# Kernel optimization log

Measured on AMD Instinct MI355X. Metric: run time of the kernel, lower is better.

Reference implementation:

```python
import jax, jax.numpy as jnp
import numpy as np

G = 17  # groups == deform_groups
EPS = 1e-5

# regular 3x3 kernel grid in homogeneous coords: rows = (dy, dx, 1), cols = 9 kernel taps (row-major)
REG = jnp.array([[-1, -1, -1, 0, 0, 0, 1, 1, 1],
                 [-1, 0, 1, -1, 0, 1, -1, 0, 1],
                 [1, 1, 1, 1, 1, 1, 1, 1, 1]], dtype=jnp.float32)
KY = jnp.array([-1, -1, -1, 0, 0, 0, 1, 1, 1], dtype=jnp.float32)
KX = jnp.array([-1, 0, 1, -1, 0, 1, -1, 0, 1], dtype=jnp.float32)


def setup_inputs() -> dict:
    key = jax.random.key(0)
    k0, k1, k2 = jax.random.split(key, 3)
    B, C, H, W = 2, 272, 128, 128
    Cg = C // G
    x = jax.random.normal(k0, (B, C, H, W), jnp.float32)
    tm_w = jax.random.normal(k1, (6 * G, Cg, 3, 3), jnp.float32) * 0.02  # offset-transform conv weight
    tm_b = jnp.zeros((6 * G,), jnp.float32)
    dc_w = jax.random.normal(k2, (C, Cg, 3, 3), jnp.float32) * 0.05     # deform conv weight (no bias)
    gamma = jnp.ones((C,), jnp.float32)
    beta = jnp.zeros((C,), jnp.float32)
    return dict(x=x, tm_w=tm_w, tm_b=tm_b, dc_w=dc_w, gamma=gamma, beta=beta)


def _deform_sample(x, dy, dx):
    """Bilinear-sample x (B,C,H,W) at per-group offsets dy,dx (B,H,W,G,9).
    Returns (B,G,Cg,9,H,W). Zero padding outside the image (mmcv semantics)."""
    B, C, H, W = x.shape
    Cg = C // G
    hh = jnp.arange(H, dtype=x.dtype)[None, :, None, None, None]
    ww = jnp.arange(W, dtype=x.dtype)[None, None, :, None, None]
    py = hh + KY + dy  # (B,H,W,G,9)
    px = ww + KX + dx
    y0 = jnp.floor(py)
    x0 = jnp.floor(px)
    wy = py - y0
    wx = px - x0
    y0i = y0.astype(jnp.int32)
    x0i = x0.astype(jnp.int32)
    x_g = x.reshape(B, G, Cg, H * W)

    def corner(yi, xi, wgt):
        valid = (yi >= 0) & (yi < H) & (xi >= 0) & (xi < W)
        lin = jnp.clip(yi, 0, H - 1) * W + jnp.clip(xi, 0, W - 1)  # (B,H,W,G,9)
        lin = lin.transpose(0, 3, 4, 1, 2).reshape(B, G, 1, 9 * H * W)
        idx = jnp.broadcast_to(lin, (B, G, Cg, 9 * H * W))
        vals = jnp.take_along_axis(x_g, idx, axis=3).reshape(B, G, Cg, 9, H, W)
        w = (wgt * valid.astype(x.dtype)).transpose(0, 3, 4, 1, 2)  # (B,G,9,H,W)
        return vals * w[:, :, None]

    samp = corner(y0i, x0i, (1 - wy) * (1 - wx))
    samp = samp + corner(y0i, x0i + 1, (1 - wy) * wx)
    samp = samp + corner(y0i + 1, x0i, wy * (1 - wx))
    samp = samp + corner(y0i + 1, x0i + 1, wy * wx)
    return samp


def _forward(x, tm_w, tm_b, dc_w, gamma, beta):
    B, C, H, W = x.shape
    Cg = C // G
    # 1) offset-transform conv (grouped 3x3, SAME)
    aff = jax.lax.conv_general_dilated(
        x, tm_w, window_strides=(1, 1), padding='SAME',
        dimension_numbers=('NCHW', 'OIHW', 'NCHW'), feature_group_count=G)
    aff = aff + tm_b[None, :, None, None]  # (B,6G,H,W)
    # faithful to torch: view(B,2,3,G,H,W).permute(0,4,5,3,1,2) @ REG
    aff = aff.reshape(B, 2, 3, G, H, W).transpose(0, 4, 5, 3, 1, 2)  # (B,H,W,G,2,3)
    off = jnp.einsum('bhwgij,jk->bhwgik', aff, REG)  # (B,H,W,G,2,9)
    # DeformConv2d reads the flattened 18 channels as interleaved (dy,dx) pairs per tap
    off = off.reshape(B, H, W, G, 18).reshape(B, H, W, G, 9, 2)
    dy, dx = off[..., 0], off[..., 1]
    # 2) deformable 3x3 conv, groups=deform_groups=G, bias=False
    samp = _deform_sample(x, dy, dx)  # (B,G,Cg,9,H,W)
    w = dc_w.reshape(G, Cg, Cg, 3 * 3)  # (g, out-in-group, in-in-group, tap)
    out = jnp.einsum('bgckhw,gock->bgohw', samp, w).reshape(B, C, H, W)
    # 3) batch norm (training-mode stats) + residual ReLU
    mean = jnp.mean(out, axis=(0, 2, 3), keepdims=True)
    var = jnp.var(out, axis=(0, 2, 3), keepdims=True)
    out = (out - mean) * jax.lax.rsqrt(var + EPS)
    out = out * gamma[None, :, None, None] + beta[None, :, None, None]
    return jax.nn.relu(out + x)


def reference(x, tm_w, tm_b, dc_w, gamma, beta):
    return _forward(x, tm_w, tm_b, dc_w, gamma, beta)
```

## Files before the change

kernel.cpp:

```cpp
#include <hip/hip_runtime.h>
#include <math.h>

#define BB 2
#define CC 272
#define GG 17
#define CG 16
#define HH 128
#define WW 128
#define HWX (HH*WW)
#define AFFC 102
#define NSLAB (BB*GG)
#define TILES_PER_SLAB 64
#define NWG (NSLAB*TILES_PER_SLAB)
#define WGPX (NWG/8)
#define PSTR ((size_t)NSLAB*HWX*4)

typedef float f4nt __attribute__((ext_vector_type(4)));
typedef unsigned u4nt __attribute__((ext_vector_type(4)));
typedef _Float16 h2 __attribute__((ext_vector_type(2)));

__device__ __forceinline__ h2 bch(unsigned u) { return __builtin_bit_cast(h2, u); }
__device__ __forceinline__ unsigned hpk(float a, float b) {
    return __builtin_bit_cast(unsigned, __builtin_amdgcn_cvt_pkrtz(a, b));
}
__device__ __forceinline__ h2 hbc(float a) {
    return __builtin_bit_cast(h2, __builtin_amdgcn_cvt_pkrtz(a, a));
}

#if __has_builtin(__builtin_amdgcn_fdot2)
#define FDOT2(A, B, C) __builtin_amdgcn_fdot2((A), (B), (C), false)
#else
#define FDOT2(A, B, C) fmaf((float)(A).x, (float)(B).x, fmaf((float)(A).y, (float)(B).y, (C)))
#endif

__device__ __forceinline__ unsigned f2bf(float f) {
    unsigned u = __float_as_uint(f);
    return (u + 0x7fffu + ((u >> 16) & 1u)) >> 16;
}
__device__ __forceinline__ float bflo(unsigned u) { return __uint_as_float(u << 16); }
__device__ __forceinline__ float bfhi(unsigned u) { return __uint_as_float(u & 0xffff0000u); }

__global__ __launch_bounds__(256) void wt_kernel(
    const float* __restrict__ dc_w, const float* __restrict__ tm_w,
    unsigned* __restrict__ dc_wh, unsigned* __restrict__ tm_wh)
{
    int i = blockIdx.x * 256 + threadIdx.x;
    if (i < GG * 8 * 9 * CG) {
        int oc = i & 15, t = (i >> 4) % 9, cp = (i / 144) % 8, g = i / 1152;
        float w0 = dc_w[((size_t)(g * 16 + oc) * 16 + 2 * cp) * 9 + t];
        float w1 = dc_w[((size_t)(g * 16 + oc) * 16 + 2 * cp + 1) * 9 + t];
        dc_wh[i] = hpk(w0, w1);
    }
    if (i < GG * 6 * 9 * 8) {
        int cp = i & 7, t = (i >> 3) % 9, j = (i / 72) % 6, ig = i / 432;
        float w0 = tm_w[((size_t)(ig * 6 + j) * 16 + 2 * cp) * 9 + t];
        float w1 = tm_w[((size_t)(ig * 6 + j) * 16 + 2 * cp + 1) * 9 + t];
        tm_wh[i] = hpk(w0, w1);
    }
}

__global__ __launch_bounds__(256) void transpose_kernel(
    const float* __restrict__ x, unsigned* __restrict__ xt)
{
    __shared__ float tile[CG][WW + 1];
    const int h = blockIdx.x & (HH - 1);
    const int g = (blockIdx.x >> 7) % GG;
    const int b = blockIdx.x / (GG * HH);
    const int tid = threadIdx.x;
    const float* src = x + (size_t)(b * CC + g * CG) * HWX + h * WW;
    for (int i = tid; i < CG * WW; i += 256) {
        int c = i >> 7, w = i & (WW - 1);
        tile[c][w] = src[(size_t)c * HWX + w];
    }
    __syncthreads();
    const size_t rowbase = ((size_t)(b * GG + g) * HWX + h * WW) * 4;
    unsigned* d0 = xt + rowbase;
    unsigned* d1 = xt + PSTR + rowbase;
    for (int i = tid; i < 4 * WW; i += 256) {
        int w = i >> 2, c4 = i & 3;
        d0[(size_t)w * 4 + c4] = hpk(tile[2 * c4][w],     tile[2 * c4 + 1][w]);
        d1[(size_t)w * 4 + c4] = hpk(tile[8 + 2 * c4][w], tile[8 + 2 * c4 + 1][w]);
    }
}

__global__ __launch_bounds__(256) void aff_conv_kernel(
    const unsigned* __restrict__ xt, const unsigned* __restrict__ tm_wh,
    const float* __restrict__ tm_b, float* __restrict__ aff)
{
    const int ig = blockIdx.y;
    const int b = blockIdx.z;
    const int tid = threadIdx.x;

    const int p = blockIdx.x * 256 + tid;
    const int h = p >> 7, w = p & (WW - 1);
    const unsigned* xb0 = xt + (size_t)(b * GG + ig) * HWX * 4;
    const unsigned* xb1 = xb0 + PSTR;
    const unsigned* wbh = tm_wh + (size_t)ig * (6 * 9 * 8);

    float acc[6];
#pragma unroll
    for (int j = 0; j < 6; ++j) acc[j] = 0.f;

#pragma unroll 1
    for (int t = 0; t < 9; ++t) {
        int hy = h + t / 3 - 1;
        int wx = w + t % 3 - 1;
        uint4 u0 = {0, 0, 0, 0}, u1 = {0, 0, 0, 0};
        if (hy >= 0 && hy < HH && wx >= 0 && wx < WW) {
            u0 = *(const uint4*)(xb0 + (size_t)(hy * WW + wx) * 4);
            u1 = *(const uint4*)(xb1 + (size_t)(hy * WW + wx) * 4);
        }
#pragma unroll
        for (int j = 0; j < 6; ++j) {
            const uint4* wp = (const uint4*)(wbh + (j * 9 + t) * 8);
            uint4 qa = wp[0], qb = wp[1];
            float a = acc[j];
            a = FDOT2(bch(u0.x), bch(qa.x), a); a = FDOT2(bch(u0.y), bch(qa.y), a);
            a = FDOT2(bch(u0.z), bch(qa.z), a); a = FDOT2(bch(u0.w), bch(qa.w), a);
            a = FDOT2(bch(u1.x), bch(qb.x), a); a = FDOT2(bch(u1.y), bch(qb.y), a);
            a = FDOT2(bch(u1.z), bch(qb.z), a); a = FDOT2(bch(u1.w), bch(qb.w), a);
            acc[j] = a;
        }
    }
#pragma unroll
    for (int j = 0; j < 6; ++j)
        aff[(size_t)(b * AFFC + ig * 6 + j) * HWX + p] = acc[j] + tm_b[ig * 6 + j];
}


#define MACC(T, CP, S2) { \
    const uint4* wp_ = (const uint4*)(wgh + ((CP) * 9 + (T)) * CG); \
    uint4 q0 = wp_[0], q1 = wp_[1], q2 = wp_[2], q3 = wp_[3]; \
    acc[0]  = FDOT2(S2, bch(q0.x), acc[0]);  acc[1]  = FDOT2(S2, bch(q0.y), acc[1]); \
    acc[2]  = FDOT2(S2, bch(q0.z), acc[2]);  acc[3]  = FDOT2(S2, bch(q0.w), acc[3]); \
    acc[4]  = FDOT2(S2, bch(q1.x), acc[4]);  acc[5]  = FDOT2(S2, bch(q1.y), acc[5]); \
    acc[6]  = FDOT2(S2, bch(q1.z), acc[6]);  acc[7]  = FDOT2(S2, bch(q1.w), acc[7]); \
    acc[8]  = FDOT2(S2, bch(q2.x), acc[8]);  acc[9]  = FDOT2(S2, bch(q2.y), acc[9]); \
    acc[10] = FDOT2(S2, bch(q2.z), acc[10]); acc[11] = FDOT2(S2, bch(q2.w), acc[11]); \
    acc[12] = FDOT2(S2, bch(q3.x), acc[12]); acc[13] = FDOT2(S2, bch(q3.y), acc[13]); \
    acc[14] = FDOT2(S2, bch(q3.z), acc[14]); acc[15] = FDOT2(S2, bch(q3.w), acc[15]); }

#define SEM(T, CP, UA, UB, UC, UD) { \
    h2 s2 = bch(UA) * W00 + bch(UB) * W01 + bch(UC) * W10 + bch(UD) * W11; \
    MACC(T, CP, s2) }

#define TAP(T, I0, K0, I1, K1) { \
    float dy = ((I0) ? a10 : a00) * (float)((K0) / 3 - 1) \
             + ((I0) ? a11 : a01) * (float)((K0) % 3 - 1) + ((I0) ? a12 : a02); \
    float dx = ((I1) ? a10 : a00) * (float)((K1) / 3 - 1) \
             + ((I1) ? a11 : a01) * (float)((K1) % 3 - 1) + ((I1) ? a12 : a02); \
    float py = (float)(h + (T) / 3 - 1) + dy; \
    float px = (float)(w + (T) % 3 - 1) + dx; \
    float y0f = floorf(py), x0f = floorf(px); \
    float wy = py - y0f, wx = px - x0f; \
    int y0 = (int)y0f, x0 = (int)x0f; \
    int y1 = y0 + 1, x1 = x0 + 1; \
    bool vy0 = (y0 >= 0) && (y0 < HH), vy1 = (y1 >= 0) && (y1 < HH); \
    bool vx0 = (x0 >= 0) && (x0 < WW), vx1 = (x1 >= 0) && (x1 < WW); \
    int y0c = min(max(y0, 0), HH - 1), y1c = min(max(y1, 0), HH - 1); \
    int x0c = min(max(x0, 0), WW - 1), x1c = min(max(x1, 0), WW - 1); \
    float w00 = (vy0 && vx0) ? (1.f - wy) * (1.f - wx) : 0.f; \
    float w01 = (vy0 && vx1) ? (1.f - wy) * wx : 0.f; \
    float w10 = (vy1 && vx0) ? wy * (1.f - wx) : 0.f; \
    float w11 = (vy1 && vx1) ? wy * wx : 0.f; \
    h2 W00 = hbc(w00), W01 = hbc(w01), W10 = hbc(w10), W11 = hbc(w11); \
    int l00 = y0c * WW + x0c, l01 = y0c * WW + x1c; \
    int l10 = y1c * WW + x0c, l11 = y1c * WW + x1c; \
    uint4 A0 = *(const uint4*)(xb0 + (size_t)l00 * 4); \
    uint4 A1 = *(const uint4*)(xb1 + (size_t)l00 * 4); \
    uint4 B0 = *(const uint4*)(xb0 + (size_t)l01 * 4); \
    uint4 B1 = *(const uint4*)(xb1 + (size_t)l01 * 4); \
    uint4 C0 = *(const uint4*)(xb0 + (size_t)l10 * 4); \
    uint4 C1 = *(const uint4*)(xb1 + (size_t)l10 * 4); \
    uint4 D0 = *(const uint4*)(xb0 + (size_t)l11 * 4); \
    uint4 D1 = *(const uint4*)(xb1 + (size_t)l11 * 4); \
    SEM(T, 0, A0.x, B0.x, C0.x, D0.x) SEM(T, 1, A0.y, B0.y, C0.y, D0.y) \
    SEM(T, 2, A0.z, B0.z, C0.z, D0.z) SEM(T, 3, A0.w, B0.w, C0.w, D0.w) \
    SEM(T, 4, A1.x, B1.x, C1.x, D1.x) SEM(T, 5, A1.y, B1.y, C1.y, D1.y) \
    SEM(T, 6, A1.z, B1.z, C1.z, D1.z) SEM(T, 7, A1.w, B1.w, C1.w, D1.w) }

__global__ __launch_bounds__(256, 6) void deform_kernel(
    const unsigned* __restrict__ xt, const unsigned* __restrict__ dc_wh,
    const float* __restrict__ aff_buf, unsigned* __restrict__ pre,
    float* __restrict__ stat_sum, float* __restrict__ stat_sqs)
{
    __shared__ float red[CG][4][2];

    const int bid = blockIdx.x;
    const int work = (bid & 7) * WGPX + (bid >> 3);
    const int slab = work / TILES_PER_SLAB;
    const int tile = work % TILES_PER_SLAB;
    const int b = slab / GG;
    const int g = slab % GG;

    const int tid = threadIdx.y * 16 + threadIdx.x;
    const int h = (tile >> 3) * 16 + threadIdx.y;
    const int w = (tile & 7) * 16 + threadIdx.x;

    const float* ab = aff_buf + (size_t)b * AFFC * HWX + h * WW + w;
    float a00 = __builtin_nontemporal_load(ab + (size_t)(0 * 51 + 0 * 17 + g) * HWX);
    float a01 = __builtin_nontemporal_load(ab + (size_t)(0 * 51 + 1 * 17 + g) * HWX);
    float a02 = __builtin_nontemporal_load(ab + (size_t)(0 * 51 + 2 * 17 + g) * HWX);
    float a10 = __builtin_nontemporal_load(ab + (size_t)(1 * 51 + 0 * 17 + g) * HWX);
    float a11 = __builtin_nontemporal_load(ab + (size_t)(1 * 51 + 1 * 17 + g) * HWX);
    float a12 = __builtin_nontemporal_load(ab + (size_t)(1 * 51 + 2 * 17 + g) * HWX);

    const unsigned* xb0 = xt + (size_t)(b * GG + g) * HWX * 4;
    const unsigned* xb1 = xb0 + PSTR;
    const unsigned* wgh = dc_wh + (size_t)g * (8 * 9 * CG);

    float acc[CG];
#pragma unroll
    for (int oc = 0; oc < CG; ++oc) acc[oc] = 0.f;

    TAP(0, 0, 0, 0, 1)
    TAP(1, 0, 2, 0, 3)
    TAP(2, 0, 4, 0, 5)
    TAP(3, 0, 6, 0, 7)
    TAP(4, 0, 8, 1, 0)
    TAP(5, 1, 1, 1, 2)
    TAP(6, 1, 3, 1, 4)
    TAP(7, 1, 5, 1, 6)
    TAP(8, 1, 7, 1, 8)

    unsigned pk[8];
#pragma unroll
    for (int k = 0; k < 8; ++k)
        pk[k] = f2bf(acc[2 * k]) | (f2bf(acc[2 * k + 1]) << 16);
    {
        u4nt q0 = {pk[0], pk[1], pk[2], pk[3]};
        u4nt q1 = {pk[4], pk[5], pk[6], pk[7]};
        u4nt* pp = (u4nt*)(pre + ((size_t)slab * HWX + h * WW + w) * (CG / 2));
        __builtin_nontemporal_store(q0, pp);
        __builtin_nontemporal_store(q1, pp + 1);
    }

    const int lane = tid & 63, wave = tid >> 6;
#pragma unroll
    for (int oc = 0; oc < CG; ++oc) {
        float s = acc[oc], q = acc[oc] * acc[oc];
#pragma unroll
        for (int off = 32; off > 0; off >>= 1) {
            s += __shfl_down(s, off);
            q += __shfl_down(q, off);
        }
        if (lane == 0) { red[oc][wave][0] = s; red[oc][wave][1] = q; }
    }
    __syncthreads();
    if (tid < CG) {
        float s = red[tid][0][0] + red[tid][1][0] + red[tid][2][0] + red[tid][3][0];
        float q = red[tid][0][1] + red[tid][1][1] + red[tid][2][1] + red[tid][3][1];
        int ch = g * CG + tid;
        atomicAdd(&stat_sum[ch], s);
        atomicAdd(&stat_sqs[ch], q);
    }
}

__global__ __launch_bounds__(256) void bn_res_relu_kernel(
    const unsigned* __restrict__ pre, const float* __restrict__ x,
    const float* __restrict__ ssum, const float* __restrict__ ssqs,
    const float* __restrict__ gamma, const float* __restrict__ beta,
    float* __restrict__ out)
{
    const int blk = blockIdx.x;
    const int slab = blk >> 4;
    const int chunk = blk & 15;
    const int b = slab / GG, g = slab % GG;
    const int px0 = chunk * 1024 + threadIdx.x * 4;

    const float n = (float)(BB * HWX);
    float sc[16], sh[16];
#pragma unroll
    for (int oc = 0; oc < 16; ++oc) {
        int ch = g * CG + oc;
        float mean = ssum[ch] / n;
        float var = ssqs[ch] / n - mean * mean;
        float s = rsqrtf(var + 1e-5f) * gamma[ch];
        sc[oc] = s;
        sh[oc] = fmaf(-mean, s, beta[ch]);
    }

    const uint4* pp = (const uint4*)(pre + ((size_t)slab * HWX + px0) * (CG / 2));
    unsigned Pu[32];
#pragma unroll
    for (int k = 0; k < 8; ++k) {
        uint4 v = pp[k];
        Pu[4 * k] = v.x; Pu[4 * k + 1] = v.y; Pu[4 * k + 2] = v.z; Pu[4 * k + 3] = v.w;
    }
    const float* xb = x + (size_t)(b * CC + g * CG) * HWX + px0;
    float* ob = out + (size_t)(b * CC + g * CG) * HWX + px0;

#pragma unroll
    for (int oc = 0; oc < 16; ++oc) {
        f4nt xv = __builtin_nontemporal_load((const f4nt*)(xb + (size_t)oc * HWX));
        f4nt r;
        float p0, p1, p2, p3;
        {
            unsigned u0 = Pu[0 * 8 + (oc >> 1)], u1 = Pu[1 * 8 + (oc >> 1)];
            unsigned u2 = Pu[2 * 8 + (oc >> 1)], u3 = Pu[3 * 8 + (oc >> 1)];
            p0 = (oc & 1) ? bfhi(u0) : bflo(u0);
            p1 = (oc & 1) ? bfhi(u1) : bflo(u1);
            p2 = (oc & 1) ? bfhi(u2) : bflo(u2);
            p3 = (oc & 1) ? bfhi(u3) : bflo(u3);
        }
        r.x = fmaxf(fmaf(p0, sc[oc], sh[oc]) + xv.x, 0.f);
        r.y = fmaxf(fmaf(p1, sc[oc], sh[oc]) + xv.y, 0.f);
        r.z = fmaxf(fmaf(p2, sc[oc], sh[oc]) + xv.z, 0.f);
        r.w = fmaxf(fmaf(p3, sc[oc], sh[oc]) + xv.w, 0.f);
        __builtin_nontemporal_store(r, (f4nt*)(ob + (size_t)oc * HWX));
    }
}

extern "C" void kernel_launch(void* const* d_in, const int* in_sizes, int n_in,
                              void* d_out, int out_size, void* d_ws, size_t ws_size,
                              hipStream_t stream)
{
    const float* x     = (const float*)d_in[0];
    const float* tm_w  = (const float*)d_in[1];
    const float* tm_b  = (const float*)d_in[2];
    const float* dc_w  = (const float*)d_in[3];
    const float* gamma = (const float*)d_in[4];
    const float* beta  = (const float*)d_in[5];
    float* out = (float*)d_out;

    float* ws = (float*)d_ws;
    float* stat_sum = ws;
    float* stat_sqs = ws + CC;
    unsigned* dc_wh = (unsigned*)(ws + 2048);
    unsigned* tm_wh = dc_wh + 19712;
    float* aff = (float*)(tm_wh + 7424);
    unsigned* xtb = (unsigned*)(aff + (size_t)BB * AFFC * HWX);
    unsigned* preb = xtb + 2 * PSTR;

    (void)hipMemsetAsync(stat_sum, 0, 2 * CC * sizeof(float), stream);

    wt_kernel<<<dim3(77), dim3(256), 0, stream>>>(dc_w, tm_w, dc_wh, tm_wh);
    transpose_kernel<<<dim3(BB * GG * HH), dim3(256), 0, stream>>>(x, xtb);
    aff_conv_kernel<<<dim3(HWX / 256, GG, BB), dim3(256), 0, stream>>>(xtb, tm_wh, tm_b, aff);
    deform_kernel<<<dim3(NWG), dim3(16, 16), 0, stream>>>(
        xtb, dc_wh, aff, preb, stat_sum, stat_sqs);
    bn_res_relu_kernel<<<dim3(NSLAB * 16), dim3(256), 0, stream>>>(
        preb, x, stat_sum, stat_sqs, gamma, beta, out);
}
```

Baseline: 121.0 us.

## Compute two pixels per thread in deform kernel to amortize weight loads

Each deform-kernel thread now handles two pixels 16 columns apart, sharing each weight uint4 load across both accumulator sets. Tiles per slab are halved so the grid shrinks, and the launch bound drops to 4 waves to make room for the extra registers. The affine conv tap loop is also partially unrolled. The gain is fewer weight loads per output and more independent gathers in flight per thread. The cost is much higher register pressure and occupancy, plus fewer workgroups to cover the device.

```diff
diff --git a/kernel.cpp b/kernel.cpp
--- a/kernel.cpp
+++ b/kernel.cpp
@@ -10,7 +10,7 @@
 #define HWX (HH*WW)
 #define AFFC 102
 #define NSLAB (BB*GG)
-#define TILES_PER_SLAB 64
+#define TILES_PER_SLAB 32
 #define NWG (NSLAB*TILES_PER_SLAB)
 #define WGPX (NWG/8)
 #define PSTR ((size_t)NSLAB*HWX*4)
@@ -101,7 +101,7 @@
 #pragma unroll
     for (int j = 0; j < 6; ++j) acc[j] = 0.f;
 
-#pragma unroll 1
+#pragma unroll 3
     for (int t = 0; t < 9; ++t) {
         int hy = h + t / 3 - 1;
         int wx = w + t % 3 - 1;
@@ -144,42 +144,53 @@
     h2 s2 = bch(UA) * W00 + bch(UB) * W01 + bch(UC) * W10 + bch(UD) * W11; \
     MACC(T, CP, s2) }
 
-#define TAP(T, I0, K0, I1, K1) { \
-    float dy = ((I0) ? a10 : a00) * (float)((K0) / 3 - 1) \
-             + ((I0) ? a11 : a01) * (float)((K0) % 3 - 1) + ((I0) ? a12 : a02); \
-    float dx = ((I1) ? a10 : a00) * (float)((K1) / 3 - 1) \
-             + ((I1) ? a11 : a01) * (float)((K1) % 3 - 1) + ((I1) ? a12 : a02); \
-    float py = (float)(h + (T) / 3 - 1) + dy; \
-    float px = (float)(w + (T) % 3 - 1) + dx; \
-    float y0f = floorf(py), x0f = floorf(px); \
-    float wy = py - y0f, wx = px - x0f; \
-    int y0 = (int)y0f, x0 = (int)x0f; \
-    int y1 = y0 + 1, x1 = x0 + 1; \
-    bool vy0 = (y0 >= 0) && (y0 < HH), vy1 = (y1 >= 0) && (y1 < HH); \
-    bool vx0 = (x0 >= 0) && (x0 < WW), vx1 = (x1 >= 0) && (x1 < WW); \
-    int y0c = min(max(y0, 0), HH - 1), y1c = min(max(y1, 0), HH - 1); \
-    int x0c = min(max(x0, 0), WW - 1), x1c = min(max(x1, 0), WW - 1); \
-    float w00 = (vy0 && vx0) ? (1.f - wy) * (1.f - wx) : 0.f; \
-    float w01 = (vy0 && vx1) ? (1.f - wy) * wx : 0.f; \
-    float w10 = (vy1 && vx0) ? wy * (1.f - wx) : 0.f; \
-    float w11 = (vy1 && vx1) ? wy * wx : 0.f; \
-    h2 W00 = hbc(w00), W01 = hbc(w01), W10 = hbc(w10), W11 = hbc(w11); \
-    int l00 = y0c * WW + x0c, l01 = y0c * WW + x1c; \
-    int l10 = y1c * WW + x0c, l11 = y1c * WW + x1c; \
-    uint4 A0 = *(const uint4*)(xb0 + (size_t)l00 * 4); \
-    uint4 A1 = *(const uint4*)(xb1 + (size_t)l00 * 4); \
-    uint4 B0 = *(const uint4*)(xb0 + (size_t)l01 * 4); \
-    uint4 B1 = *(const uint4*)(xb1 + (size_t)l01 * 4); \
-    uint4 C0 = *(const uint4*)(xb0 + (size_t)l10 * 4); \
-    uint4 C1 = *(const uint4*)(xb1 + (size_t)l10 * 4); \
-    uint4 D0 = *(const uint4*)(xb0 + (size_t)l11 * 4); \
-    uint4 D1 = *(const uint4*)(xb1 + (size_t)l11 * 4); \
-    SEM(T, 0, A0.x, B0.x, C0.x, D0.x) SEM(T, 1, A0.y, B0.y, C0.y, D0.y) \
-    SEM(T, 2, A0.z, B0.z, C0.z, D0.z) SEM(T, 3, A0.w, B0.w, C0.w, D0.w) \
-    SEM(T, 4, A1.x, B1.x, C1.x, D1.x) SEM(T, 5, A1.y, B1.y, C1.y, D1.y) \
-    SEM(T, 6, A1.z, B1.z, C1.z, D1.z) SEM(T, 7, A1.w, B1.w, C1.w, D1.w) }
-
-__global__ __launch_bounds__(256, 6) void deform_kernel(
+template<int T, int I0, int K0, int I1, int K1>
+__device__ __forceinline__ void tap_px(
+    const unsigned* __restrict__ xb0, const unsigned* __restrict__ xb1,
+    const unsigned* __restrict__ wgh,
+    float a00, float a01, float a02, float a10, float a11, float a12,
+    int h, int w, float (&acc)[16])
+{
+    float dy = (I0 ? a10 : a00) * (float)(K0 / 3 - 1)
+             + (I0 ? a11 : a01) * (float)(K0 % 3 - 1) + (I0 ? a12 : a02);
+    float dx = (I1 ? a10 : a00) * (float)(K1 / 3 - 1)
+             + (I1 ? a11 : a01) * (float)(K1 % 3 - 1) + (I1 ? a12 : a02);
+    float py = (float)(h + T / 3 - 1) + dy;
+    float px = (float)(w + T % 3 - 1) + dx;
+    float y0f = floorf(py), x0f = floorf(px);
+    float wy = py - y0f, wx = px - x0f;
+    int y0 = (int)y0f, x0 = (int)x0f;
+    int y1 = y0 + 1, x1 = x0 + 1;
+    bool vy0 = (y0 >= 0) && (y0 < HH), vy1 = (y1 >= 0) && (y1 < HH);
+    bool vx0 = (x0 >= 0) && (x0 < WW), vx1 = (x1 >= 0) && (x1 < WW);
+    int y0c = min(max(y0, 0), HH - 1), y1c = min(max(y1, 0), HH - 1);
+    int x0c = min(max(x0, 0), WW - 1), x1c = min(max(x1, 0), WW - 1);
+    float w00 = (vy0 && vx0) ? (1.f - wy) * (1.f - wx) : 0.f;
+    float w01 = (vy0 && vx1) ? (1.f - wy) * wx : 0.f;
+    float w10 = (vy1 && vx0) ? wy * (1.f - wx) : 0.f;
+    float w11 = (vy1 && vx1) ? wy * wx : 0.f;
+    h2 W00 = hbc(w00), W01 = hbc(w01), W10 = hbc(w10), W11 = hbc(w11);
+    int l00 = y0c * WW + x0c, l01 = y0c * WW + x1c;
+    int l10 = y1c * WW + x0c, l11 = y1c * WW + x1c;
+    uint4 A0 = *(const uint4*)(xb0 + (size_t)l00 * 4);
+    uint4 A1 = *(const uint4*)(xb1 + (size_t)l00 * 4);
+    uint4 B0 = *(const uint4*)(xb0 + (size_t)l01 * 4);
+    uint4 B1 = *(const uint4*)(xb1 + (size_t)l01 * 4);
+    uint4 C0 = *(const uint4*)(xb0 + (size_t)l10 * 4);
+    uint4 C1 = *(const uint4*)(xb1 + (size_t)l10 * 4);
+    uint4 D0 = *(const uint4*)(xb0 + (size_t)l11 * 4);
+    uint4 D1 = *(const uint4*)(xb1 + (size_t)l11 * 4);
+    SEM(T, 0, A0.x, B0.x, C0.x, D0.x) SEM(T, 1, A0.y, B0.y, C0.y, D0.y)
+    SEM(T, 2, A0.z, B0.z, C0.z, D0.z) SEM(T, 3, A0.w, B0.w, C0.w, D0.w)
+    SEM(T, 4, A1.x, B1.x, C1.x, D1.x) SEM(T, 5, A1.y, B1.y, C1.y, D1.y)
+    SEM(T, 6, A1.z, B1.z, C1.z, D1.z) SEM(T, 7, A1.w, B1.w, C1.w, D1.w)
+}
+
+#define TAP2(T, I0, K0, I1, K1) \
+    tap_px<T, I0, K0, I1, K1>(xb0, xb1, wgh, a00, a01, a02, a10, a11, a12, h, w0, acc0); \
+    tap_px<T, I0, K0, I1, K1>(xb0, xb1, wgh, b00, b01, b02, b10, b11, b12, h, w1, acc1);
+
+__global__ __launch_bounds__(256, 4) void deform_kernel(
     const unsigned* __restrict__ xt, const unsigned* __restrict__ dc_wh,
     const float* __restrict__ aff_buf, unsigned* __restrict__ pre,
     float* __restrict__ stat_sum, float* __restrict__ stat_sqs)
@@ -194,51 +205,70 @@
     const int g = slab % GG;
 
     const int tid = threadIdx.y * 16 + threadIdx.x;
-    const int h = (tile >> 3) * 16 + threadIdx.y;
-    const int w = (tile & 7) * 16 + threadIdx.x;
-
-    const float* ab = aff_buf + (size_t)b * AFFC * HWX + h * WW + w;
-    float a00 = __builtin_nontemporal_load(ab + (size_t)(0 * 51 + 0 * 17 + g) * HWX);
-    float a01 = __builtin_nontemporal_load(ab + (size_t)(0 * 51 + 1 * 17 + g) * HWX);
-    float a02 = __builtin_nontemporal_load(ab + (size_t)(0 * 51 + 2 * 17 + g) * HWX);
-    float a10 = __builtin_nontemporal_load(ab + (size_t)(1 * 51 + 0 * 17 + g) * HWX);
-    float a11 = __builtin_nontemporal_load(ab + (size_t)(1 * 51 + 1 * 17 + g) * HWX);
-    float a12 = __builtin_nontemporal_load(ab + (size_t)(1 * 51 + 2 * 17 + g) * HWX);
+    const int h = (tile >> 2) * 16 + threadIdx.y;
+    const int w0 = (tile & 3) * 32 + threadIdx.x;
+    const int w1 = w0 + 16;
+
+    const float* ab = aff_buf + (size_t)b * AFFC * HWX + h * WW;
+    float a00 = __builtin_nontemporal_load(ab + (size_t)(0 * 51 + 0 * 17 + g) * HWX + w0);
+    float a01 = __builtin_nontemporal_load(ab + (size_t)(0 * 51 + 1 * 17 + g) * HWX + w0);
+    float a02 = __builtin_nontemporal_load(ab + (size_t)(0 * 51 + 2 * 17 + g) * HWX + w0);
+    float a10 = __builtin_nontemporal_load(ab + (size_t)(1 * 51 + 0 * 17 + g) * HWX + w0);
+    float a11 = __builtin_nontemporal_load(ab + (size_t)(1 * 51 + 1 * 17 + g) * HWX + w0);
+    float a12 = __builtin_nontemporal_load(ab + (size_t)(1 * 51 + 2 * 17 + g) * HWX + w0);
+    float b00 = __builtin_nontemporal_load(ab + (size_t)(0 * 51 + 0 * 17 + g) * HWX + w1);
+    float b01 = __builtin_nontemporal_load(ab + (size_t)(0 * 51 + 1 * 17 + g) * HWX + w1);
+    float b02 = __builtin_nontemporal_load(ab + (size_t)(0 * 51 + 2 * 17 + g) * HWX + w1);
+    float b10 = __builtin_nontemporal_load(ab + (size_t)(1 * 51 + 0 * 17 + g) * HWX + w1);
+    float b11 = __builtin_nontemporal_load(ab + (size_t)(1 * 51 + 1 * 17 + g) * HWX + w1);
+    float b12 = __builtin_nontemporal_load(ab + (size_t)(1 * 51 + 2 * 17 + g) * HWX + w1);
 
     const unsigned* xb0 = xt + (size_t)(b * GG + g) * HWX * 4;
     const unsigned* xb1 = xb0 + PSTR;
     const unsigned* wgh = dc_wh + (size_t)g * (8 * 9 * CG);
 
-    float acc[CG];
-#pragma unroll
-    for (int oc = 0; oc < CG; ++oc) acc[oc] = 0.f;
-
-    TAP(0, 0, 0, 0, 1)
-    TAP(1, 0, 2, 0, 3)
-    TAP(2, 0, 4, 0, 5)
-    TAP(3, 0, 6, 0, 7)
-    TAP(4, 0, 8, 1, 0)
-    TAP(5, 1, 1, 1, 2)
-    TAP(6, 1, 3, 1, 4)
-    TAP(7, 1, 5, 1, 6)
-    TAP(8, 1, 7, 1, 8)
-
-    unsigned pk[8];
-#pragma unroll
-    for (int k = 0; k < 8; ++k)
-        pk[k] = f2bf(acc[2 * k]) | (f2bf(acc[2 * k + 1]) << 16);
+    float acc0[CG], acc1[CG];
+#pragma unroll
+    for (int oc = 0; oc < CG; ++oc) { acc0[oc] = 0.f; acc1[oc] = 0.f; }
+
+    TAP2(0, 0, 0, 0, 1)
+    TAP2(1, 0, 2, 0, 3)
+    TAP2(2, 0, 4, 0, 5)
+    TAP2(3, 0, 6, 0, 7)
+    TAP2(4, 0, 8, 1, 0)
+    TAP2(5, 1, 1, 1, 2)
+    TAP2(6, 1, 3, 1, 4)
+    TAP2(7, 1, 5, 1, 6)
+    TAP2(8, 1, 7, 1, 8)
+
     {
+        unsigned pk[8];
+#pragma unroll
+        for (int k = 0; k < 8; ++k)
+            pk[k] = f2bf(acc0[2 * k]) | (f2bf(acc0[2 * k + 1]) << 16);
         u4nt q0 = {pk[0], pk[1], pk[2], pk[3]};
         u4nt q1 = {pk[4], pk[5], pk[6], pk[7]};
-        u4nt* pp = (u4nt*)(pre + ((size_t)slab * HWX + h * WW + w) * (CG / 2));
+        u4nt* pp = (u4nt*)(pre + ((size_t)slab * HWX + h * WW + w0) * (CG / 2));
         __builtin_nontemporal_store(q0, pp);
         __builtin_nontemporal_store(q1, pp + 1);
     }
+    {
+        unsigned pk[8];
+#pragma unroll
+        for (int k = 0; k < 8; ++k)
+            pk[k] = f2bf(acc1[2 * k]) | (f2bf(acc1[2 * k + 1]) << 16);
+        u4nt q0 = {pk[0], pk[1], pk[2], pk[3]};
+        u4nt q1 = {pk[4], pk[5], pk[6], pk[7]};
+        u4nt* pp = (u4nt*)(pre + ((size_t)slab * HWX + h * WW + w1) * (CG / 2));
+        __builtin_nontemporal_store(q0, pp);
+        __builtin_nontemporal_store(q1, pp + 1);
+    }
 
     const int lane = tid & 63, wave = tid >> 6;
 #pragma unroll
     for (int oc = 0; oc < CG; ++oc) {
-        float s = acc[oc], q = acc[oc] * acc[oc];
+        float s = acc0[oc] + acc1[oc];
+        float q = acc0[oc] * acc0[oc] + acc1[oc] * acc1[oc];
 #pragma unroll
         for (int off = 32; off > 0; off >>= 1) {
             s += __shfl_down(s, off);
```

Measured after the change: 122.6 us. About the same (+1.3%).
